# Performance work log

Hardware: AMD Instinct MI355X
Metric: run time of the kernel (lower is better)

## Reference

```python
import jax, jax.numpy as jnp
import numpy as np

B, N, F_IN, F_HID, F_EMB, H, L_DIM = 8, 1024, 128, 128, 128, 8, 2


def _xavier(key, shape, fan_in, fan_out):
    lim = np.sqrt(6.0 / (fan_in + fan_out))
    return jax.random.uniform(key, shape, jnp.float32, -lim, lim)


def setup_inputs() -> dict:
    key = jax.random.key(0)
    ks = jax.random.split(key, 16)
    x = jax.random.normal(ks[0], (B, N, F_IN), jnp.float32)
    # sparse 0/1 adjacency with self loops (avoids fully-masked softmax rows)
    adj = (jax.random.uniform(ks[1], (B, N, N)) < 0.05).astype(jnp.float32)
    adj = jnp.maximum(adj, jnp.eye(N, dtype=jnp.float32)[None])
    def gat_params(k, f_in, f_out):
        k1, k2, k3 = jax.random.split(k, 3)
        return (_xavier(k1, (H, f_in, f_out), f_in, f_out),
                _xavier(k2, (H, f_out, 1), f_out, 1),
                _xavier(k3, (H, f_out, 1), f_out, 1),
                jnp.zeros((f_out,), jnp.float32))
    w1, as1, ad1, b1 = gat_params(ks[2], F_IN, F_HID)
    w2, as2, ad2, b2 = gat_params(ks[3], F_HID, F_HID)
    w3, as3, ad3, b3 = gat_params(ks[4], F_HID, F_EMB)
    pred_in = F_HID * 2 + F_EMB  # hidden*(num_layers-1)+embedding, concat=True
    pw = _xavier(ks[5], (pred_in, L_DIM), pred_in, L_DIM)
    pb = jnp.zeros((L_DIM,), jnp.float32)
    return {"x": x, "adj": adj,
            "w1": w1, "as1": as1, "ad1": ad1, "b1": b1,
            "w2": w2, "as2": as2, "ad2": ad2, "b2": b2,
            "w3": w3, "as3": as3, "ad3": ad3, "b3": b3,
            "pw": pw, "pb": pb}


def gat_layer(h, adj, w, a_src, a_dst, bias):
    # h: [B,N,f_in] -> h_prime: [B,H,N,f_out]
    hp = jnp.einsum('bnf,hfo->bhno', h, w)
    t = jnp.tanh(hp)
    s = jnp.einsum('bhno,hoi->bhni', t, a_src)[..., 0]  # [B,H,N]
    d = jnp.einsum('bhno,hoi->bhni', t, a_dst)[..., 0]  # [B,H,N]
    scores = s[:, :, :, None] + d[:, :, None, :]        # [B,H,N,N]
    scores = jnp.where(scores >= 0, scores, 0.2 * scores)  # LeakyReLU(0.2)
    scores = jnp.where(adj[:, None, :, :] > 0, scores, -jnp.inf)
    attn = jax.nn.softmax(scores, axis=-1)  # dropout disabled (eval mode)
    out = jnp.einsum('bhnm,bhmo->bhno', attn, hp) + bias
    return out.mean(axis=1)  # merge heads -> [B,N,f_out]


def reference(x, adj, w1, as1, ad1, b1, w2, as2, ad2, b2, w3, as3, ad3, b3, pw, pb):
    x1 = jax.nn.relu(gat_layer(x, adj, w1, as1, ad1, b1))
    x2 = jax.nn.relu(gat_layer(x1, adj, w2, as2, ad2, b2))
    x3 = gat_layer(x2, adj, w3, as3, ad3, b3)
    x_all = jnp.concatenate([x1, x2, x3], axis=2)  # [B,N,pred_in]
    pooled = jnp.max(x_all, axis=1)                # max over nodes -> [B,pred_in]
    return pooled @ pw + pb                        # [B,label_dim]
```

## Files before the change

### kernel.cpp

```cpp
#include <hip/hip_runtime.h>
#include <hip/hip_fp16.h>

#define BB 8
#define NN 1024
#define FF 128
#define HH 8

typedef _Float16 f16;
typedef f16  f16x8 __attribute__((ext_vector_type(8)));
typedef f16  f16x4 __attribute__((ext_vector_type(4)));
typedef float f32x4 __attribute__((ext_vector_type(4)));

#define L2E 1.44269504f

__global__ void k_pre(const float* __restrict__ x, f16* __restrict__ x16a,
                      const float* __restrict__ w1, const float* __restrict__ w2,
                      const float* __restrict__ w3, f16* __restrict__ wB,
                      const float* __restrict__ adj, unsigned* __restrict__ am){
  int bid = blockIdx.x, t = threadIdx.x;
  if (bid < 512){
    int i = (bid*256 + t)*8;
    float4 a = *(const float4*)(x+i), b = *(const float4*)(x+i+4);
    f16x8 v;
    v[0]=(f16)a.x; v[1]=(f16)a.y; v[2]=(f16)a.z; v[3]=(f16)a.w;
    v[4]=(f16)b.x; v[5]=(f16)b.y; v[6]=(f16)b.z; v[7]=(f16)b.w;
    *(f16x8*)(x16a+i) = v;
  } else if (bid < 704){
    int e = (bid-512)*256 + t;
    int fc = e & 15, c = (e>>4)&127, h = (e>>11)&7, l = e>>14;
    const float* w = (l==0) ? w1 : ((l==1) ? w2 : w3);
    f16x8 v;
    #pragma unroll
    for(int j=0;j<8;j++) v[j] = (f16)w[(h*128 + fc*8 + j)*128 + c];
    *(f16x8*)(wB + (((l*8+h)*16 + fc)*128 + c)*8) = v;
  } else {
    int wv = t >> 6, lane = t & 63;
    int r = (bid-704)*4 + wv;
    const float* row = adj + (long)r*1024;
    for(int g=0; g<16; g++){
      float v = __builtin_nontemporal_load(row + g*64 + lane);
      unsigned long long mb = __ballot(v > 0.0f);
      if (lane == 0){
        am[r*32 + 2*g]   = (unsigned)mb;
        am[r*32 + 2*g+1] = (unsigned)(mb >> 32);
      }
    }
  }
}

__global__ __launch_bounds__(256,2) void k_hp(
    const f16* __restrict__ xin,
    const f16* __restrict__ wBl,
    const float* __restrict__ asrc, const float* __restrict__ adst,
    f16* __restrict__ hpB,
    float* __restrict__ sarr, float* __restrict__ darr)
{
  __shared__ f16 xs[128*136];
  __shared__ float asl[128], adl[128];
  int t = threadIdx.x;
  int bid = blockIdx.x;
  int it = bid & 7, h = (bid>>3)&7, b = bid>>6;
  int i0 = it*128;
  {
    const f16* src = xin + (long)(b*1024 + i0)*128;
    int fc = t & 15, r0 = t >> 4;
    #pragma unroll
    for(int p=0;p<8;p++){
      int r = r0 + p*16;
      f16x8 v = *(const f16x8*)(src + r*128 + fc*8);
      *(f16x8*)(xs + r*136 + fc*8) = v;
    }
  }
  if (t < 128){ asl[t] = asrc[h*128+t]; adl[t] = adst[h*128+t]; }
  __syncthreads();

  int lane = t & 63, wv = t>>6, wr = wv>>1, wc = wv&1;
  int mq = lane & 15, quad = lane >> 4;
  f32x4 acc[4][4];
  #pragma unroll
  for(int a=0;a<4;a++)
    #pragma unroll
    for(int c=0;c<4;c++) acc[a][c] = (f32x4){0.f,0.f,0.f,0.f};

  const f16* wh = wBl + h*16*128*8;
  #pragma unroll
  for(int ks=0; ks<4; ks++){
    f16x8 af[4], bf[4];
    #pragma unroll
    for(int mt=0; mt<4; mt++)
      af[mt] = *(const f16x8*)(xs + (wr*64 + mt*16 + mq)*136 + ks*32 + quad*8);
    #pragma unroll
    for(int nt=0; nt<4; nt++){
      int c  = wc*64 + nt*16 + mq;
      int fc = ks*4 + quad;
      bf[nt] = *(const f16x8*)(wh + (fc*128 + c)*8);
    }
    #pragma unroll
    for(int mt=0; mt<4; mt++)
      #pragma unroll
      for(int nt=0; nt<4; nt++)
        acc[mt][nt] = __builtin_amdgcn_mfma_f32_16x16x32_f16(af[mt], bf[nt], acc[mt][nt], 0,0,0);
  }
  __syncthreads();
  f16* tt = xs;
  f16* hpb = hpB + (long)(b*8+h)*128*128*8;
  #pragma unroll
  for(int mt=0; mt<4; mt++){
    #pragma unroll
    for(int nt=0; nt<4; nt++){
      int c = wc*64 + nt*16 + mq;
      f16x4 pk;
      #pragma unroll
      for(int rg=0; rg<4; rg++){
        float v = acc[mt][nt][rg];
        pk[rg] = (f16)v;
        int il = wr*64 + mt*16 + quad*4 + rg;
        float e2 = __expf(2.0f*v);
        float th = 1.0f - 2.0f*__builtin_amdgcn_rcpf(e2 + 1.0f);
        tt[il*136 + c] = (f16)th;
      }
      int il0 = wr*64 + mt*16 + quad*4;
      int inode = i0 + il0;
      *(f16x4*)(hpb + ((long)(inode>>3)*128 + c)*8 + (inode&7)) = pk;
    }
  }
  __syncthreads();
  {
    int r = t>>1, hf = t&1;
    float s_p = 0.f, d_p = 0.f;
    #pragma unroll
    for(int q=0;q<8;q++){
      f16x8 tv = *(const f16x8*)(tt + r*136 + hf*64 + q*8);
      #pragma unroll
      for(int j=0;j<8;j++){
        float tvf = (float)tv[j];
        int c = hf*64 + q*8 + j;
        s_p = fmaf(tvf, asl[c], s_p);
        d_p = fmaf(tvf, adl[c], d_p);
      }
    }
    s_p += __shfl_xor(s_p, 1);
    d_p += __shfl_xor(d_p, 1);
    if (hf == 0){
      sarr[(b*8+h)*1024 + i0 + r] = s_p;
      darr[(b*8+h)*1024 + i0 + r] = d_p;
    }
  }
}

__global__ __launch_bounds__(256,4) void k_attn(
    const f16* __restrict__ hpB,
    const float* __restrict__ sarr, const float* __restrict__ darr,
    const unsigned* __restrict__ am,
    f16* __restrict__ part,
    float* __restrict__ zpart)
{
  __shared__ float ddl[512];
  __shared__ float wred[4];
  __shared__ f16 Pl[2][128*40];
  int t = threadIdx.x;
  int bid = blockIdx.x;
  int bh = bid & 63, q = bid >> 6;
  int jh = q & 1, it = q >> 1;
  int i0 = it*128, j0 = jh*512;
  int b = bh >> 3;

  {
    float4 v = *(const float4*)(darr + bh*1024 + t*4);
    float mx = fmaxf(fmaxf(v.x,v.y), fmaxf(v.z,v.w));
    #pragma unroll
    for(int o=1;o<64;o<<=1) mx = fmaxf(mx, __shfl_xor(mx, o));
    if ((t&63)==0) wred[t>>6] = mx;
    int base = t*4 - j0;
    if (base >= 0 && base < 512){
      float4 s = make_float4(v.x*L2E, v.y*L2E, v.z*L2E, v.w*L2E);
      *(float4*)(ddl + base) = s;
    }
  }
  __syncthreads();
  float Dml = fmaxf(fmaxf(wred[0],wred[1]), fmaxf(wred[2],wred[3])) * L2E;

  int prow = t>>1, pjg = t&1;
  float srowl = sarr[bh*1024 + i0 + prow] * L2E;
  float ml = srowl + Dml;
  float mrowl = fmaxf(ml, 0.2f*ml);
  const unsigned* amrow = am + ((long)(b*1024 + i0 + prow))*32 + jh*16;

  int lane = t&63, wv = t>>6, wr = wv>>1, wc = wv&1;
  int mq = lane&15, quad = lane>>4;
  const f16* hpb = hpB + (long)bh*128*128*8;
  f32x4 acc[4][4];
  #pragma unroll
  for(int a=0;a<4;a++)
    #pragma unroll
    for(int c=0;c<4;c++) acc[a][c] = (f32x4){0.f,0.f,0.f,0.f};
  float zacc = 0.f;
  f16x8 zerov = (f16x8){0,0,0,0,0,0,0,0};

  f16* myp0 = Pl[0] + prow*40 + pjg*16;
  f16* myp1 = Pl[1] + prow*40 + pjg*16;

  auto compP = [&](int jtn, f16* myp){
    *(f16x8*)(myp)     = zerov;
    *(f16x8*)(myp + 8) = zerov;
    unsigned word = (amrow[jtn] >> (pjg*16)) & 0xffffu;
    const float* dloc = ddl + jtn*32 + pjg*16;
    while(word){
      int j = __builtin_ctz(word);
      word &= word - 1u;
      float xl  = srowl + dloc[j];
      float scl = fmaxf(xl, 0.2f*xl);
      float e   = __builtin_amdgcn_exp2f(scl - mrowl);
      zacc += e;
      myp[j] = (f16)e;
    }
  };

  compP(0, myp0);

  #pragma unroll 2
  for(int jt=0; jt<16; jt++){
    f16x8 bf[4];
    #pragma unroll
    for(int nt=0;nt<4;nt++){
      int c  = wc*64 + nt*16 + mq;
      int jc = jh*64 + jt*4 + quad;
      bf[nt] = *(const f16x8*)(hpb + (jc*128 + c)*8);
    }
    __syncthreads();
    const f16* Pb = Pl[jt&1];
    f16x8 af[4];
    #pragma unroll
    for(int mt=0;mt<4;mt++)
      af[mt] = *(const f16x8*)(Pb + (wr*64 + mt*16 + mq)*40 + quad*8);
    if (jt < 15) compP(jt+1, ((jt+1)&1) ? myp1 : myp0);
    #pragma unroll
    for(int mt=0;mt<4;mt++)
      #pragma unroll
      for(int nt=0;nt<4;nt++)
        acc[mt][nt] = __builtin_amdgcn_mfma_f32_16x16x32_f16(af[mt], bf[nt], acc[mt][nt], 0,0,0);
  }
  zacc += __shfl_xor(zacc, 1);
  if (pjg == 0) __builtin_nontemporal_store(zacc, zpart + (jh*64 + bh)*1024 + i0 + prow);
  f16* pout = part + ((long)(jh*64 + bh)*1024 + i0)*128;
  #pragma unroll
  for(int mt=0;mt<4;mt++){
    #pragma unroll
    for(int nt=0;nt<4;nt++){
      int c = wc*64 + nt*16 + mq;
      #pragma unroll
      for(int rg=0;rg<4;rg++){
        int il = wr*64 + mt*16 + quad*4 + rg;
        __builtin_nontemporal_store((f16)acc[mt][nt][rg], pout + il*128 + c);
      }
    }
  }
}

__global__ void k_fin(const f16* __restrict__ part, const float* __restrict__ zp,
                      const float* __restrict__ bias,
                      f16* __restrict__ x16, float* __restrict__ pmax, int do_relu){
  __shared__ float pm[16][128];
  int t = threadIdx.x;
  int idx = blockIdx.x*256 + t;
  int c8 = idx & 15, n = (idx>>4)&1023, b = idx>>14;
  float s[8];
  #pragma unroll
  for(int j=0;j<8;j++) s[j] = 0.f;
  #pragma unroll
  for(int h=0;h<8;h++){
    int bh = b*8 + h;
    float zi = 0.125f / (zp[bh*1024 + n] + zp[65536 + bh*1024 + n]);
    f16x8 p0 = __builtin_nontemporal_load((const f16x8*)(part + ((long)bh*1024 + n)*128 + c8*8));
    f16x8 p1 = __builtin_nontemporal_load((const f16x8*)(part + ((long)(64+bh)*1024 + n)*128 + c8*8));
    #pragma unroll
    for(int j=0;j<8;j++) s[j] = fmaf((float)p0[j] + (float)p1[j], zi, s[j]);
  }
  f16x8 h8;
  float ov[8];
  #pragma unroll
  for(int j=0;j<8;j++){
    float v = s[j] + bias[c8*8 + j];
    if (do_relu) v = fmaxf(v, 0.f);
    ov[j] = v;
    h8[j] = (f16)v;
  }
  if (x16) *(f16x8*)(x16 + ((long)(b*1024+n))*128 + c8*8) = h8;
  #pragma unroll
  for(int j=0;j<8;j++) pm[n&15][c8*8+j] = ov[j];
  __syncthreads();
  if (t < 128){
    float m = pm[0][t];
    #pragma unroll
    for(int r=1;r<16;r++) m = fmaxf(m, pm[r][t]);
    pmax[blockIdx.x*128 + t] = m;
  }
}

__global__ void k_pool2(const float* __restrict__ pmax, const float* __restrict__ pw,
                        const float* __restrict__ pb, float* __restrict__ out){
  __shared__ float pl[384];
  int b = blockIdx.x, t = threadIdx.x;
  for(int f = t; f < 384; f += 256){
    int l = f >> 7, c = f & 127;
    const float* p = pmax + l*65536 + b*64*128 + c;
    float mx = -3.4e38f;
    #pragma unroll 8
    for(int k=0;k<64;k++) mx = fmaxf(mx, p[k*128]);
    pl[f] = mx;
  }
  __syncthreads();
  if (t < 64){
    float a0 = 0.f, a1 = 0.f;
    #pragma unroll
    for(int k=0;k<6;k++){
      int f = t + 64*k;
      float v = pl[f];
      a0 = fmaf(v, pw[f*2],   a0);
      a1 = fmaf(v, pw[f*2+1], a1);
    }
    #pragma unroll
    for(int o=1;o<64;o<<=1){ a0 += __shfl_xor(a0,o); a1 += __shfl_xor(a1,o); }
    if (t == 0){ out[b*2] = a0 + pb[0]; out[b*2+1] = a1 + pb[1]; }
  }
}

extern "C" void kernel_launch(void* const* d_in, const int* in_sizes, int n_in,
                              void* d_out, int out_size, void* d_ws, size_t ws_size,
                              hipStream_t stream) {
  const float* x   = (const float*)d_in[0];
  const float* adj = (const float*)d_in[1];
  const float* w1  = (const float*)d_in[2];
  const float* as1 = (const float*)d_in[3];
  const float* ad1 = (const float*)d_in[4];
  const float* b1  = (const float*)d_in[5];
  const float* w2  = (const float*)d_in[6];
  const float* as2 = (const float*)d_in[7];
  const float* ad2 = (const float*)d_in[8];
  const float* b2  = (const float*)d_in[9];
  const float* w3  = (const float*)d_in[10];
  const float* as3 = (const float*)d_in[11];
  const float* ad3 = (const float*)d_in[12];
  const float* b3  = (const float*)d_in[13];
  const float* pw  = (const float*)d_in[14];
  const float* pb  = (const float*)d_in[15];

  char* ws = (char*)d_ws;
  f16*      x16a = (f16*)ws;                 ws += (size_t)1048576*2;
  f16*      x16b = (f16*)ws;                 ws += (size_t)1048576*2;
  f16*      wB   = (f16*)ws;                 ws += (size_t)393216*2;
  unsigned* am   = (unsigned*)ws;            ws += (size_t)8*1024*32*4;
  f16*      hpB  = (f16*)ws;                 ws += (size_t)8*8*1024*128*2;
  float*    sarr = (float*)ws;               ws += (size_t)65536*4;
  float*    darr = (float*)ws;               ws += (size_t)65536*4;
  f16*      part = (f16*)ws;                 ws += (size_t)2*64*1024*128*2;
  float*    zp   = (float*)ws;               ws += (size_t)2*65536*4;
  float*    pmax = (float*)ws;               ws += (size_t)3*512*128*4;

  k_pre<<<2752, 256, 0, stream>>>(x, x16a, w1, w2, w3, wB, adj, am);

  k_hp  <<<512, 256, 0, stream>>>(x16a, wB,            as1, ad1, hpB, sarr, darr);
  k_attn<<<1024,256, 0, stream>>>(hpB, sarr, darr, am, part, zp);
  k_fin <<<512, 256, 0, stream>>>(part, zp, b1, x16b, pmax,           1);
  k_hp  <<<512, 256, 0, stream>>>(x16b, wB + 131072,   as2, ad2, hpB, sarr, darr);
  k_attn<<<1024,256, 0, stream>>>(hpB, sarr, darr, am, part, zp);
  k_fin <<<512, 256, 0, stream>>>(part, zp, b2, x16a, pmax + 65536,   1);
  k_hp  <<<512, 256, 0, stream>>>(x16a, wB + 262144,   as3, ad3, hpB, sarr, darr);
  k_attn<<<1024,256, 0, stream>>>(hpB, sarr, darr, am, part, zp);
  k_fin <<<512, 256, 0, stream>>>(part, zp, b3, nullptr, pmax + 131072, 0);

  k_pool2<<<8, 256, 0, stream>>>(pmax, pw, pb, (float*)d_out);
}
```

Baseline: 304.1 us.

## Drop split-K in attention kernel, normalize in-kernel, prefetch B fragments

The attention kernel no longer splits the neighbor dimension into two halves. Each block now covers all 1024 columns and divides by the softmax denominator itself, so the partial-output and partial-denominator buffers and their reads in the finalize kernel go away. The loop also software-prefetches the next hp fragment and adjacency word one iteration ahead. The trade-off is half as many blocks (512) with a lower occupancy hint, and a serial loop twice as long per block.

Measured after the change: 272.7 us. 10.3% less time.

```diff
diff --git a/kernel.cpp b/kernel.cpp
--- a/kernel.cpp
+++ b/kernel.cpp
@@ -49,11 +49,9 @@
 }
 
 __global__ __launch_bounds__(256,2) void k_hp(
-    const f16* __restrict__ xin,
-    const f16* __restrict__ wBl,
+    const f16* __restrict__ xin, const f16* __restrict__ wBl,
     const float* __restrict__ asrc, const float* __restrict__ adst,
-    f16* __restrict__ hpB,
-    float* __restrict__ sarr, float* __restrict__ darr)
+    f16* __restrict__ hpB, float* __restrict__ sarr, float* __restrict__ darr)
 {
   __shared__ f16 xs[128*136];
   __shared__ float asl[128], adl[128];
@@ -148,21 +146,20 @@
   }
 }
 
-__global__ __launch_bounds__(256,4) void k_attn(
+__global__ __launch_bounds__(256,2) void k_attn(
     const f16* __restrict__ hpB,
     const float* __restrict__ sarr, const float* __restrict__ darr,
     const unsigned* __restrict__ am,
-    f16* __restrict__ part,
-    float* __restrict__ zpart)
+    f16* __restrict__ part)
 {
-  __shared__ float ddl[512];
+  __shared__ float ddl[1024];
   __shared__ float wred[4];
+  __shared__ float zin[128];
   __shared__ f16 Pl[2][128*40];
   int t = threadIdx.x;
   int bid = blockIdx.x;
-  int bh = bid & 63, q = bid >> 6;
-  int jh = q & 1, it = q >> 1;
-  int i0 = it*128, j0 = jh*512;
+  int bh = bid & 63, it = bid >> 6;
+  int i0 = it*128;
   int b = bh >> 3;
 
   {
@@ -171,11 +168,7 @@
     #pragma unroll
     for(int o=1;o<64;o<<=1) mx = fmaxf(mx, __shfl_xor(mx, o));
     if ((t&63)==0) wred[t>>6] = mx;
-    int base = t*4 - j0;
-    if (base >= 0 && base < 512){
-      float4 s = make_float4(v.x*L2E, v.y*L2E, v.z*L2E, v.w*L2E);
-      *(float4*)(ddl + base) = s;
-    }
+    *(float4*)(ddl + t*4) = make_float4(v.x*L2E, v.y*L2E, v.z*L2E, v.w*L2E);
   }
   __syncthreads();
   float Dml = fmaxf(fmaxf(wred[0],wred[1]), fmaxf(wred[2],wred[3])) * L2E;
@@ -184,7 +177,7 @@
   float srowl = sarr[bh*1024 + i0 + prow] * L2E;
   float ml = srowl + Dml;
   float mrowl = fmaxf(ml, 0.2f*ml);
-  const unsigned* amrow = am + ((long)(b*1024 + i0 + prow))*32 + jh*16;
+  const unsigned* amrow = am + ((long)(b*1024 + i0 + prow))*32;
 
   int lane = t&63, wv = t>>6, wr = wv>>1, wc = wv&1;
   int mq = lane&15, quad = lane>>4;
@@ -200,10 +193,10 @@
   f16* myp0 = Pl[0] + prow*40 + pjg*16;
   f16* myp1 = Pl[1] + prow*40 + pjg*16;
 
-  auto compP = [&](int jtn, f16* myp){
+  auto compP = [&](int jtn, f16* myp, unsigned w32){
     *(f16x8*)(myp)     = zerov;
     *(f16x8*)(myp + 8) = zerov;
-    unsigned word = (amrow[jtn] >> (pjg*16)) & 0xffffu;
+    unsigned word = (w32 >> (pjg*16)) & 0xffffu;
     const float* dloc = ddl + jtn*32 + pjg*16;
     while(word){
       int j = __builtin_ctz(word);
@@ -216,16 +209,27 @@
     }
   };
 
-  compP(0, myp0);
+  compP(0, myp0, amrow[0]);
+  unsigned wNext = amrow[1];
+  f16x8 bfc[4];
+  #pragma unroll
+  for(int nt=0;nt<4;nt++){
+    int c = wc*64 + nt*16 + mq;
+    bfc[nt] = *(const f16x8*)(hpb + (quad*128 + c)*8);
+  }
 
   #pragma unroll 2
-  for(int jt=0; jt<16; jt++){
-    f16x8 bf[4];
-    #pragma unroll
-    for(int nt=0;nt<4;nt++){
-      int c  = wc*64 + nt*16 + mq;
-      int jc = jh*64 + jt*4 + quad;
-      bf[nt] = *(const f16x8*)(hpb + (jc*128 + c)*8);
+  for(int jt=0; jt<32; jt++){
+    f16x8 bfn[4];
+    unsigned wNN = 0;
+    if (jt < 31){
+      #pragma unroll
+      for(int nt=0;nt<4;nt++){
+        int c  = wc*64 + nt*16 + mq;
+        int jc = (jt+1)*4 + quad;
+        bfn[nt] = *(const f16x8*)(hpb + (jc*128 + c)*8);
+      }
+      if (jt < 30) wNN = amrow[jt+2];
     }
     __syncthreads();
     const f16* Pb = Pl[jt&1];
@@ -233,16 +237,22 @@
     #pragma unroll
     for(int mt=0;mt<4;mt++)
       af[mt] = *(const f16x8*)(Pb + (wr*64 + mt*16 + mq)*40 + quad*8);
-    if (jt < 15) compP(jt+1, ((jt+1)&1) ? myp1 : myp0);
+    if (jt < 31) compP(jt+1, ((jt+1)&1) ? myp1 : myp0, wNext);
     #pragma unroll
     for(int mt=0;mt<4;mt++)
       #pragma unroll
       for(int nt=0;nt<4;nt++)
-        acc[mt][nt] = __builtin_amdgcn_mfma_f32_16x16x32_f16(af[mt], bf[nt], acc[mt][nt], 0,0,0);
-  }
+        acc[mt][nt] = __builtin_amdgcn_mfma_f32_16x16x32_f16(af[mt], bfc[nt], acc[mt][nt], 0,0,0);
+    #pragma unroll
+    for(int nt=0;nt<4;nt++) bfc[nt] = bfn[nt];
+    wNext = wNN;
+  }
+
   zacc += __shfl_xor(zacc, 1);
-  if (pjg == 0) __builtin_nontemporal_store(zacc, zpart + (jh*64 + bh)*1024 + i0 + prow);
-  f16* pout = part + ((long)(jh*64 + bh)*1024 + i0)*128;
+  if (pjg == 0) zin[prow] = 0.125f / zacc;
+  __syncthreads();
+
+  f16* pout = part + ((long)bh*1024 + i0)*128;
   #pragma unroll
   for(int mt=0;mt<4;mt++){
     #pragma unroll
@@ -251,14 +261,13 @@
       #pragma unroll
       for(int rg=0;rg<4;rg++){
         int il = wr*64 + mt*16 + quad*4 + rg;
-        __builtin_nontemporal_store((f16)acc[mt][nt][rg], pout + il*128 + c);
-      }
-    }
-  }
-}
-
-__global__ void k_fin(const f16* __restrict__ part, const float* __restrict__ zp,
-                      const float* __restrict__ bias,
+        pout[il*128 + c] = (f16)(acc[mt][nt][rg] * zin[il]);
+      }
+    }
+  }
+}
+
+__global__ void k_fin(const f16* __restrict__ part, const float* __restrict__ bias,
                       f16* __restrict__ x16, float* __restrict__ pmax, int do_relu){
   __shared__ float pm[16][128];
   int t = threadIdx.x;
@@ -269,12 +278,9 @@
   for(int j=0;j<8;j++) s[j] = 0.f;
   #pragma unroll
   for(int h=0;h<8;h++){
-    int bh = b*8 + h;
-    float zi = 0.125f / (zp[bh*1024 + n] + zp[65536 + bh*1024 + n]);
-    f16x8 p0 = __builtin_nontemporal_load((const f16x8*)(part + ((long)bh*1024 + n)*128 + c8*8));
-    f16x8 p1 = __builtin_nontemporal_load((const f16x8*)(part + ((long)(64+bh)*1024 + n)*128 + c8*8));
-    #pragma unroll
-    for(int j=0;j<8;j++) s[j] = fmaf((float)p0[j] + (float)p1[j], zi, s[j]);
+    f16x8 p0 = *(const f16x8*)(part + ((long)(b*8+h)*1024 + n)*128 + c8*8);
+    #pragma unroll
+    for(int j=0;j<8;j++) s[j] += (float)p0[j];
   }
   f16x8 h8;
   float ov[8];
@@ -353,21 +359,20 @@
   f16*      hpB  = (f16*)ws;                 ws += (size_t)8*8*1024*128*2;
   float*    sarr = (float*)ws;               ws += (size_t)65536*4;
   float*    darr = (float*)ws;               ws += (size_t)65536*4;
-  f16*      part = (f16*)ws;                 ws += (size_t)2*64*1024*128*2;
-  float*    zp   = (float*)ws;               ws += (size_t)2*65536*4;
+  f16*      part = (f16*)ws;                 ws += (size_t)64*1024*128*2;
   float*    pmax = (float*)ws;               ws += (size_t)3*512*128*4;
 
   k_pre<<<2752, 256, 0, stream>>>(x, x16a, w1, w2, w3, wB, adj, am);
 
   k_hp  <<<512, 256, 0, stream>>>(x16a, wB,            as1, ad1, hpB, sarr, darr);
-  k_attn<<<1024,256, 0, stream>>>(hpB, sarr, darr, am, part, zp);
-  k_fin <<<512, 256, 0, stream>>>(part, zp, b1, x16b, pmax,           1);
+  k_attn<<<512, 256, 0, stream>>>(hpB, sarr, darr, am, part);
+  k_fin <<<512, 256, 0, stream>>>(part, b1, x16b, pmax,           1);
   k_hp  <<<512, 256, 0, stream>>>(x16b, wB + 131072,   as2, ad2, hpB, sarr, darr);
-  k_attn<<<1024,256, 0, stream>>>(hpB, sarr, darr, am, part, zp);
-  k_fin <<<512, 256, 0, stream>>>(part, zp, b2, x16a, pmax + 65536,   1);
+  k_attn<<<512, 256, 0, stream>>>(hpB, sarr, darr, am, part);
+  k_fin <<<512, 256, 0, stream>>>(part, b2, x16a, pmax + 65536,   1);
   k_hp  <<<512, 256, 0, stream>>>(x16a, wB + 262144,   as3, ad3, hpB, sarr, darr);
-  k_attn<<<1024,256, 0, stream>>>(hpB, sarr, darr, am, part, zp);
-  k_fin <<<512, 256, 0, stream>>>(part, zp, b3, nullptr, pmax + 131072, 0);
+  k_attn<<<512, 256, 0, stream>>>(hpB, sarr, darr, am, part);
+  k_fin <<<512, 256, 0, stream>>>(part, b3, nullptr, pmax + 131072, 0);
 
   k_pool2<<<8, 256, 0, stream>>>(pmax, pw, pb, (float*)d_out);
 }
```
